# Optimization experiments

Measured on AMD Instinct MI355X. Metric: run time of the kernel, lower is better.

## Reference

```python
import jax, jax.numpy as jnp
import numpy as np

H_HEADS = 32
KV_HEADS = 8
HEAD_DIM = 64  # hidden // num_heads = 2048 // 32


def setup_inputs() -> dict:
    key = jax.random.key(0)
    ks = jax.random.split(key, 5)
    B, T, hidden = 2, 2048, 2048
    kv_dim = KV_HEADS * HEAD_DIM
    s = 0.02
    return {
        "x": jax.random.normal(ks[0], (B, T, hidden), dtype=jnp.float32),
        "Wq": jax.random.normal(ks[1], (hidden, hidden), dtype=jnp.float32) * s,
        "Wk": jax.random.normal(ks[2], (hidden, kv_dim), dtype=jnp.float32) * s,
        "Wv": jax.random.normal(ks[3], (hidden, kv_dim), dtype=jnp.float32) * s,
        "Wo": jax.random.normal(ks[4], (hidden, hidden), dtype=jnp.float32) * s,
    }


def reference(x, Wq, Wk, Wv, Wo):
    B, T, hidden = x.shape
    h, kv, d = H_HEADS, KV_HEADS, HEAD_DIM
    g = h // kv  # GQA group size
    scale = d ** (-0.5)

    # projections
    q = (x @ Wq).reshape(B, T, h, d).transpose(0, 2, 1, 3)        # [B,h,T,d]
    k = (x @ Wk).reshape(B, T, kv, d).transpose(0, 2, 1, 3)      # [B,kv,T,d]
    v = (x @ Wv).reshape(B, T, kv, d).transpose(0, 2, 1, 3)      # [B,kv,T,d]

    # native GQA broadcast: group q heads by their shared kv head
    # (equivalent math to torch repeat_interleave on k/v)
    qg = q.reshape(B, kv, g, T, d)                                # [B,kv,g,T,d]
    scores = jnp.einsum("bkgtd,bksd->bkgts", qg, k) * scale       # [B,kv,g,T,T]
    attn = jax.nn.softmax(scores, axis=-1)
    og = jnp.einsum("bkgts,bksd->bkgtd", attn, v)                 # [B,kv,g,T,d]
    out = og.reshape(B, h, T, d).transpose(0, 2, 1, 3).reshape(B, T, h * d)
    return out @ Wo
```

## Files before the change

kernel.cpp:

```cpp
#include <hip/hip_runtime.h>

#define AS1 __attribute__((address_space(1)))
#define AS3 __attribute__((address_space(3)))

typedef unsigned short u16;
typedef unsigned int u32;
typedef __attribute__((ext_vector_type(8))) _Float16 half8;
typedef __attribute__((ext_vector_type(2))) _Float16 half2v;
typedef __attribute__((ext_vector_type(4))) u16 u16x4;
typedef __attribute__((ext_vector_type(4))) u32 u32x4;
typedef __attribute__((ext_vector_type(4))) float f32x4;
typedef __attribute__((ext_vector_type(16))) float f32x16;

__device__ __forceinline__ u16 f2h(float f) {
    _Float16 h = (_Float16)f;
    return __builtin_bit_cast(u16, h);
}

__device__ __forceinline__ u32 pk2h(float a, float b) {
    return __builtin_bit_cast(u32, __builtin_amdgcn_cvt_pkrtz(a, b));
}

__device__ __forceinline__ float fexp2(float x) {
#if __has_builtin(__builtin_amdgcn_exp2f)
    return __builtin_amdgcn_exp2f(x);
#else
    return __expf(x * 0.69314718055994531f);
#endif
}

__device__ __forceinline__ float dot2acc(u32 w, float acc) {
#if __has_builtin(__builtin_amdgcn_fdot2)
    half2v ones = { (_Float16)1.f, (_Float16)1.f };
    return __builtin_amdgcn_fdot2(__builtin_bit_cast(half2v, w), ones, acc, false);
#else
    half2v p = __builtin_bit_cast(half2v, w);
    return acc + (float)p[0] + (float)p[1];
#endif
}

__device__ __forceinline__ void plswap(u32& a, u32& b) {
    asm("v_permlane32_swap_b32 %0, %1" : "+v"(a), "+v"(b));
}

__device__ __forceinline__ void async16(const void* g, void* l) {
    __builtin_amdgcn_global_load_lds((AS1 void*)g, (AS3 void*)l, 16, 0, 0);
}


__global__ void cast_f32_to_f16(const float* __restrict__ in, u16* __restrict__ out) {
    int i = (blockIdx.x * 256 + threadIdx.x) * 4;
    float4 v = *(const float4*)(in + i);
    u16x4 o = { f2h(v.x), f2h(v.y), f2h(v.z), f2h(v.w) };
    *(u16x4*)(out + i) = o;
}

__global__ void transpose_cast(const float* __restrict__ in, u16* __restrict__ out,
                               int K, int N, float scale) {
    __shared__ float tile[32][33];
    int nb = blockIdx.x * 32, kb = blockIdx.y * 32;
    int tx = threadIdx.x & 31, ty = threadIdx.x >> 5;
#pragma unroll
    for (int r = ty; r < 32; r += 8)
        tile[r][tx] = in[(size_t)(kb + r) * N + nb + tx];
    __syncthreads();
#pragma unroll
    for (int r = ty; r < 32; r += 8)
        out[(size_t)(nb + r) * K + kb + tx] = f2h(tile[tx][r] * scale);
}


template <int OUTMODE>
__global__ __launch_bounds__(256, OUTMODE == 3 ? 3 : 2) void gemm_bt(
        const u16* __restrict__ A, const u16* __restrict__ Bt,
        void* __restrict__ C, void* __restrict__ C2,
        int M, int N, int K, int ldc) {
    __shared__ __align__(16) u16 As[2][128 * 32];
    __shared__ __align__(16) u16 Bs[2][128 * 32];
    const int m0 = blockIdx.x * 128, n0 = blockIdx.y * 128;
    const int wave = threadIdx.x >> 6, lane = threadIdx.x & 63;
    const int quad = lane >> 4, mm = lane & 15;
    const int wm = (wave >> 1) * 64, wn = (wave & 1) * 64;

    const int srow = wave * 16 + (lane >> 2);
    const int scol = 8 * ((lane & 3) ^ ((lane >> 3) & 3));

    const u16* ag0 = A + (size_t)(m0 + srow) * K + scol;
    const u16* ag1 = A + (size_t)(m0 + 64 + srow) * K + scol;
    const u16* bg0 = Bt + (size_t)(n0 + srow) * K + scol;
    const u16* bg1 = Bt + (size_t)(n0 + 64 + srow) * K + scol;
    const int soff = wave * 512 + lane * 8;

    f32x4 acc[4][4] = {};
    const int swz = (mm >> 1) & 3;

#define GST(buf)                                                              \
    {                                                                         \
        u16* ad = &As[buf][soff];                                             \
        u16* bd = &Bs[buf][soff];                                             \
        async16(ag0, ad);                                                     \
        async16(ag1, ad + 2048);                                              \
        async16(bg0, bd);                                                     \
        async16(bg1, bd + 2048);                                              \
        ag0 += 32; ag1 += 32; bg0 += 32; bg1 += 32;                           \
    }

    GST(0);
    int cur = 0;

    for (int k0 = 0; k0 < K; k0 += 32) {
        __syncthreads();
        if (k0 + 32 < K) GST(cur ^ 1);
        const u16* Ac = &As[cur][0];
        const u16* Bc = &Bs[cur][0];
        half8 af[4], bf[4];
#pragma unroll
        for (int i = 0; i < 4; i++)
            af[i] = *(const half8*)(Ac + (wm + i * 16 + mm) * 32 + (quad ^ swz) * 8);
#pragma unroll
        for (int i = 0; i < 4; i++)
            bf[i] = *(const half8*)(Bc + (wn + i * 16 + mm) * 32 + (quad ^ swz) * 8);
#pragma unroll
        for (int mi = 0; mi < 4; mi++)
#pragma unroll
            for (int ni = 0; ni < 4; ni++)
                acc[mi][ni] = __builtin_amdgcn_mfma_f32_16x16x32_f16(
                    af[mi], bf[ni], acc[mi][ni], 0, 0, 0);
        cur ^= 1;
    }
#undef GST

    if (OUTMODE == 0) {
        float* Cp = (float*)C;
#pragma unroll
        for (int mi = 0; mi < 4; mi++)
#pragma unroll
            for (int r = 0; r < 4; r++) {
                float* rp = Cp + (size_t)(m0 + wm + mi * 16 + quad * 4 + r) * ldc + n0 + wn + mm;
#pragma unroll
                for (int ni = 0; ni < 4; ni++) rp[ni * 16] = acc[mi][ni][r];
            }
    } else if (OUTMODE == 1) {
        u16* Cp = (u16*)C;
#pragma unroll
        for (int mi = 0; mi < 4; mi++)
#pragma unroll
            for (int r = 0; r < 4; r++) {
                u16* rp = Cp + (size_t)(m0 + wm + mi * 16 + quad * 4 + r) * ldc + n0 + wn + mm;
#pragma unroll
                for (int ni = 0; ni < 4; ni++) rp[ni * 16] = f2h(acc[mi][ni][r]);
            }
    } else if (OUTMODE == 2) {
        u16* Cp = (u16*)C;
#pragma unroll
        for (int mi = 0; mi < 4; mi++)
#pragma unroll
            for (int r = 0; r < 4; r++) {
                int row = m0 + wm + mi * 16 + quad * 4 + r;
#pragma unroll
                for (int ni = 0; ni < 4; ni++)
                    Cp[(size_t)(n0 + wn + ni * 16 + mm) * ldc + row] = f2h(acc[mi][ni][r]);
            }
    } else {
        if (n0 < 2048) {
            u16* Qp = (u16*)C;
#pragma unroll
            for (int mi = 0; mi < 4; mi++)
#pragma unroll
                for (int r = 0; r < 4; r++) {
                    u16* rp = Qp + (size_t)(m0 + wm + mi * 16 + quad * 4 + r) * 2048 + n0 + wn + mm;
#pragma unroll
                    for (int ni = 0; ni < 4; ni++) rp[ni * 16] = f2h(acc[mi][ni][r]);
                }
        } else if (n0 < 2560) {
            u16* Kp = (u16*)C2;
#pragma unroll
            for (int mi = 0; mi < 4; mi++)
#pragma unroll
                for (int r = 0; r < 4; r++) {
                    u16* rp = Kp + (size_t)(m0 + wm + mi * 16 + quad * 4 + r) * 512 + (n0 - 2048) + wn + mm;
#pragma unroll
                    for (int ni = 0; ni < 4; ni++) rp[ni * 16] = f2h(acc[mi][ni][r]);
                }
        } else {
            u16* Vp = (u16*)C2 + (size_t)4096 * 512;
#pragma unroll
            for (int mi = 0; mi < 4; mi++)
#pragma unroll
                for (int r = 0; r < 4; r++) {
                    int row = m0 + wm + mi * 16 + quad * 4 + r;
#pragma unroll
                    for (int ni = 0; ni < 4; ni++)
                        Vp[(size_t)(n0 - 2560 + wn + ni * 16 + mm) * 4096 + row] = f2h(acc[mi][ni][r]);
                }
        }
    }
}


template <int SPLIT>
__global__ __launch_bounds__(256, 4) void attn_fwd(const u16* __restrict__ Qb,
                                                   const u16* __restrict__ Kb,
                                                   const u16* __restrict__ Vtb,
                                                   u16* __restrict__ Ob,
                                                   float* __restrict__ Of0,
                                                   float* __restrict__ Of1,
                                                   float* __restrict__ Lf) {
    __shared__ __align__(16) u16 Ks[2][64 * 64];
    __shared__ __align__(16) u16 Vs[2][64 * 64];

    const int qtb = blockIdx.x, head = blockIdx.y;
    const int b = blockIdx.z & 1, sp = blockIdx.z >> 1;
    const int kvh = head >> 2;
    const int wave = threadIdx.x >> 6, lane = threadIdx.x & 63;
    const int h = lane >> 5;
    const int q32 = lane & 31;
    const int t = threadIdx.x;

    const size_t qrow0 = (size_t)b * 2048 + qtb * 128 + wave * 32;
    const int s_beg = sp * (2048 / SPLIT), s_end = s_beg + 2048 / SPLIT;

    half8 qf[4];
#pragma unroll
    for (int s = 0; s < 4; s++)
        qf[s] = *(const half8*)(Qb + (qrow0 + q32) * 2048 + head * 64 + s * 16 + h * 8);

    f32x16 accO[2] = {};
    float lpq[4] = {0.f, 0.f, 0.f, 0.f};

    const int srow = t >> 3;
    const int lch = (t & 7) ^ (srow & 7);
    const u16* kg = Kb + ((size_t)b * 2048 + srow) * 512 + kvh * 64 + lch * 8;
    const u16* vg = Vtb + ((size_t)kvh * 64 + srow) * 4096 + b * 2048 + lch * 8;

#define STAGE(buf, s0)                                                        \
    {                                                                         \
        u16* kd = &Ks[buf][t * 8];                                            \
        u16* vd = &Vs[buf][t * 8];                                            \
        async16(kg + (size_t)(s0) * 512, kd);                                 \
        async16(kg + (size_t)((s0) + 32) * 512, kd + 2048);                   \
        async16(vg + (s0), vd);                                               \
        async16(vg + (size_t)32 * 4096 + (s0), vd + 2048);                    \
    }

    int cur = 0;
    STAGE(0, s_beg);

    const int r0 = q32, r1 = 32 + q32;
    const int sw0 = (r0 & 7), sw1 = (r1 & 7);

    for (int s0 = s_beg; s0 < s_end; s0 += 64) {
        __syncthreads();
        int sn = s0 + 64;
        if (sn < s_end) STAGE(cur ^ 1, sn);

        const u16* Kc = &Ks[cur][0];
        const u16* Vc = &Vs[cur][0];
        const u16* Kr0 = Kc + r0 * 64;
        const u16* Kr1 = Kc + r1 * 64;

        f32x16 a0, a1;
#pragma unroll
        for (int i = 0; i < 16; i++) { a0[i] = -10.f; a1[i] = -10.f; }

#pragma unroll
        for (int s = 0; s < 4; s++) {
            half8 k0 = *(const half8*)(Kr0 + (((2 * s + h) ^ sw0) << 3));
            a0 = __builtin_amdgcn_mfma_f32_32x32x16_f16(k0, qf[s], a0, 0, 0, 0);
            half8 k1 = *(const half8*)(Kr1 + (((2 * s + h) ^ sw1) << 3));
            a1 = __builtin_amdgcn_mfma_f32_32x32x16_f16(k1, qf[s], a1, 0, 0, 0);
        }

        u32 w0[8];
#pragma unroll
        for (int m = 0; m < 8; m++) {
            w0[m] = pk2h(fexp2(a0[2 * m]), fexp2(a0[2 * m + 1]));
            lpq[m & 3] = dot2acc(w0[m], lpq[m & 3]);
        }

#pragma unroll
        for (int k1 = 0; k1 < 2; k1++) {
            const int ks = k1;
            u32 d0 = w0[4 * k1 + 0], d2 = w0[4 * k1 + 2];
            u32 d1 = w0[4 * k1 + 1], d3 = w0[4 * k1 + 3];
            plswap(d0, d2);
            plswap(d1, d3);
            u32x4 pd = { d0, d1, d2, d3 };
            half8 pf = __builtin_bit_cast(half8, pd);
#pragma unroll
            for (int dt = 0; dt < 2; dt++) {
                const int rv = dt * 32 + q32;
                half8 vf = *(const half8*)(&Vc[rv * 64 + (((2 * ks + h) ^ (rv & 7)) << 3)]);
                accO[dt] = __builtin_amdgcn_mfma_f32_32x32x16_f16(vf, pf, accO[dt], 0, 0, 0);
            }
        }

        u32 w1[8];
#pragma unroll
        for (int m = 0; m < 8; m++) {
            w1[m] = pk2h(fexp2(a1[2 * m]), fexp2(a1[2 * m + 1]));
            lpq[m & 3] = dot2acc(w1[m], lpq[m & 3]);
        }

#pragma unroll
        for (int k1 = 0; k1 < 2; k1++) {
            const int ks = 2 + k1;
            u32 d0 = w1[4 * k1 + 0], d2 = w1[4 * k1 + 2];
            u32 d1 = w1[4 * k1 + 1], d3 = w1[4 * k1 + 3];
            plswap(d0, d2);
            plswap(d1, d3);
            u32x4 pd = { d0, d1, d2, d3 };
            half8 pf = __builtin_bit_cast(half8, pd);
#pragma unroll
            for (int dt = 0; dt < 2; dt++) {
                const int rv = dt * 32 + q32;
                half8 vf = *(const half8*)(&Vc[rv * 64 + (((2 * ks + h) ^ (rv & 7)) << 3)]);
                accO[dt] = __builtin_amdgcn_mfma_f32_32x32x16_f16(vf, pf, accO[dt], 0, 0, 0);
            }
        }

        cur ^= 1;
    }
#undef STAGE

    float l = (lpq[0] + lpq[1]) + (lpq[2] + lpq[3]);
    l += __shfl_xor(l, 32);

    const size_t token = qrow0 + q32;
    if (SPLIT == 1) {
        float inv = 1.f / l;
#pragma unroll
        for (int dt = 0; dt < 2; dt++)
#pragma unroll
            for (int rq = 0; rq < 4; rq++) {
                u16x4 o = { f2h(accO[dt][4 * rq + 0] * inv), f2h(accO[dt][4 * rq + 1] * inv),
                            f2h(accO[dt][4 * rq + 2] * inv), f2h(accO[dt][4 * rq + 3] * inv) };
                *(u16x4*)(Ob + token * 2048 + head * 64 + dt * 32 + rq * 8 + h * 4) = o;
            }
    } else {
        float* Op = sp ? Of1 : Of0;
#pragma unroll
        for (int dt = 0; dt < 2; dt++)
#pragma unroll
            for (int rq = 0; rq < 4; rq++) {
                f32x4 o = { accO[dt][4 * rq + 0], accO[dt][4 * rq + 1],
                            accO[dt][4 * rq + 2], accO[dt][4 * rq + 3] };
                *(f32x4*)(Op + token * 2048 + head * 64 + dt * 32 + rq * 8 + h * 4) = o;
            }
        if (!h) Lf[((size_t)sp * 4096 + token) * 32 + head] = l;
    }
}


extern "C" void kernel_launch(void* const* d_in, const int* in_sizes, int n_in,
                              void* d_out, int out_size, void* d_ws, size_t ws_size,
                              hipStream_t stream) {
    (void)in_sizes; (void)n_in; (void)out_size; (void)ws_size;
    const float* x  = (const float*)d_in[0];
    const float* Wq = (const float*)d_in[1];
    const float* Wk = (const float*)d_in[2];
    const float* Wv = (const float*)d_in[3];
    const float* Wo = (const float*)d_in[4];
    float* out = (float*)d_out;

    u16* ws = (u16*)d_ws;
    u16* xb   = ws;
    u16* Wqt  = xb   + (size_t)4096 * 2048;
    u16* Wkvt = Wqt  + (size_t)2048 * 2048;
    u16* Wot  = Wkvt + (size_t)1024 * 2048;
    u16* Qb   = Wot  + (size_t)2048 * 2048;
    u16* Kb   = Qb   + (size_t)4096 * 2048;
    u16* Vtb  = Kb   + (size_t)4096 * 512;
    u16* Ob   = Vtb  + (size_t)512 * 4096;

    const float qscale = 0.125f * 1.4426950408889634f;

    cast_f32_to_f16<<<8192, 256, 0, stream>>>(x, xb);
    transpose_cast<<<dim3(64, 64), 256, 0, stream>>>(Wq, Wqt, 2048, 2048, qscale);
    transpose_cast<<<dim3(16, 64), 256, 0, stream>>>(Wk, Wkvt, 2048, 512, 1.f);
    transpose_cast<<<dim3(16, 64), 256, 0, stream>>>(Wv, Wkvt + (size_t)512 * 2048, 2048, 512, 1.f);
    transpose_cast<<<dim3(64, 64), 256, 0, stream>>>(Wo, Wot, 2048, 2048, 1.f);

    gemm_bt<3><<<dim3(32, 24), 256, 0, stream>>>(xb, Wqt, Qb, Kb, 4096, 3072, 2048, 2048);

    attn_fwd<1><<<dim3(16, 32, 2), 256, 0, stream>>>(Qb, Kb, Vtb, Ob,
                                                     nullptr, nullptr, nullptr);

    gemm_bt<0><<<dim3(32, 16), 256, 0, stream>>>(Ob, Wot, out, nullptr, 4096, 2048, 2048, 2048);
}
```

Baseline: 312.1 us.

## Split attention over keys with combine pass, merge weight transposes, add MFMA priority

Attention now runs as a two-way split over the key range, which doubles the grid to improve occupancy. Partial fp32 outputs and row sums go to the output buffer and extra workspace, and a new combine kernel merges them into fp16. The four weight transpose launches become one launch indexed by grid z. The attention kernel also raises its launch-bound occupancy hint, seeds the first score MFMA directly from a constant, and wraps the MFMA blocks in s_setprio. The split path needs enough workspace, falls back to the old path otherwise, and adds extra fp32 traffic plus a combine launch.

```diff
diff --git a/kernel.cpp b/kernel.cpp
--- a/kernel.cpp
+++ b/kernel.cpp
@@ -55,10 +55,23 @@
     *(u16x4*)(out + i) = o;
 }
 
-__global__ void transpose_cast(const float* __restrict__ in, u16* __restrict__ out,
-                               int K, int N, float scale) {
+__global__ void transpose_cast4(const float* __restrict__ Wq, const float* __restrict__ Wk,
+                                const float* __restrict__ Wv, const float* __restrict__ Wo,
+                                u16* __restrict__ Wqt, u16* __restrict__ Wkvt,
+                                u16* __restrict__ Wot, float qscale) {
     __shared__ float tile[32][33];
+    const int z = blockIdx.z;
+    const float* in;
+    u16* out;
+    int N;
+    float scale = 1.f;
+    if (z == 0)      { in = Wq; out = Wqt; N = 2048; scale = qscale; }
+    else if (z == 1) { in = Wo; out = Wot; N = 2048; }
+    else if (z == 2) { in = Wk; out = Wkvt; N = 512; }
+    else             { in = Wv; out = Wkvt + (size_t)512 * 2048; N = 512; }
+    const int K = 2048;
     int nb = blockIdx.x * 32, kb = blockIdx.y * 32;
+    if (nb >= N) return;
     int tx = threadIdx.x & 31, ty = threadIdx.x >> 5;
 #pragma unroll
     for (int r = ty; r < 32; r += 8)
@@ -199,7 +212,7 @@
 
 
 template <int SPLIT>
-__global__ __launch_bounds__(256, 4) void attn_fwd(const u16* __restrict__ Qb,
+__global__ __launch_bounds__(256, 5) void attn_fwd(const u16* __restrict__ Qb,
                                                    const u16* __restrict__ Kb,
                                                    const u16* __restrict__ Vtb,
                                                    u16* __restrict__ Ob,
@@ -228,6 +241,10 @@
     f32x16 accO[2] = {};
     float lpq[4] = {0.f, 0.f, 0.f, 0.f};
 
+    f32x16 NEG10;
+#pragma unroll
+    for (int i = 0; i < 16; i++) NEG10[i] = -10.f;
+
     const int srow = t >> 3;
     const int lch = (t & 7) ^ (srow & 7);
     const u16* kg = Kb + ((size_t)b * 2048 + srow) * 512 + kvh * 64 + lch * 8;
@@ -260,16 +277,21 @@
         const u16* Kr1 = Kc + r1 * 64;
 
         f32x16 a0, a1;
-#pragma unroll
-        for (int i = 0; i < 16; i++) { a0[i] = -10.f; a1[i] = -10.f; }
-
-#pragma unroll
-        for (int s = 0; s < 4; s++) {
+        __builtin_amdgcn_s_setprio(1);
+        {
+            half8 k0 = *(const half8*)(Kr0 + ((h ^ sw0) << 3));
+            a0 = __builtin_amdgcn_mfma_f32_32x32x16_f16(k0, qf[0], NEG10, 0, 0, 0);
+            half8 k1 = *(const half8*)(Kr1 + ((h ^ sw1) << 3));
+            a1 = __builtin_amdgcn_mfma_f32_32x32x16_f16(k1, qf[0], NEG10, 0, 0, 0);
+        }
+#pragma unroll
+        for (int s = 1; s < 4; s++) {
             half8 k0 = *(const half8*)(Kr0 + (((2 * s + h) ^ sw0) << 3));
             a0 = __builtin_amdgcn_mfma_f32_32x32x16_f16(k0, qf[s], a0, 0, 0, 0);
             half8 k1 = *(const half8*)(Kr1 + (((2 * s + h) ^ sw1) << 3));
             a1 = __builtin_amdgcn_mfma_f32_32x32x16_f16(k1, qf[s], a1, 0, 0, 0);
         }
+        __builtin_amdgcn_s_setprio(0);
 
         u32 w0[8];
 #pragma unroll
@@ -278,6 +300,7 @@
             lpq[m & 3] = dot2acc(w0[m], lpq[m & 3]);
         }
 
+        __builtin_amdgcn_s_setprio(1);
 #pragma unroll
         for (int k1 = 0; k1 < 2; k1++) {
             const int ks = k1;
@@ -294,6 +317,7 @@
                 accO[dt] = __builtin_amdgcn_mfma_f32_32x32x16_f16(vf, pf, accO[dt], 0, 0, 0);
             }
         }
+        __builtin_amdgcn_s_setprio(0);
 
         u32 w1[8];
 #pragma unroll
@@ -302,6 +326,7 @@
             lpq[m & 3] = dot2acc(w1[m], lpq[m & 3]);
         }
 
+        __builtin_amdgcn_s_setprio(1);
 #pragma unroll
         for (int k1 = 0; k1 < 2; k1++) {
             const int ks = 2 + k1;
@@ -318,6 +343,7 @@
                 accO[dt] = __builtin_amdgcn_mfma_f32_32x32x16_f16(vf, pf, accO[dt], 0, 0, 0);
             }
         }
+        __builtin_amdgcn_s_setprio(0);
 
         cur ^= 1;
     }
@@ -351,11 +377,25 @@
     }
 }
 
+__global__ void attn_combine(const float* __restrict__ Of0, const float* __restrict__ Of1,
+                             const float* __restrict__ Lf, u16* __restrict__ Ob) {
+    size_t idx = (size_t)blockIdx.x * 256 + threadIdx.x;
+    size_t token = idx >> 9;
+    int dq = (int)(idx & 511) * 4;
+    int head = dq >> 6;
+    float inv = 1.f / (Lf[token * 32 + head] + Lf[(4096 + token) * 32 + head]);
+    float4 a = *(const float4*)(Of0 + token * 2048 + dq);
+    float4 c = *(const float4*)(Of1 + token * 2048 + dq);
+    u16x4 o = { f2h((a.x + c.x) * inv), f2h((a.y + c.y) * inv),
+                f2h((a.z + c.z) * inv), f2h((a.w + c.w) * inv) };
+    *(u16x4*)(Ob + token * 2048 + dq) = o;
+}
+
 
 extern "C" void kernel_launch(void* const* d_in, const int* in_sizes, int n_in,
                               void* d_out, int out_size, void* d_ws, size_t ws_size,
                               hipStream_t stream) {
-    (void)in_sizes; (void)n_in; (void)out_size; (void)ws_size;
+    (void)in_sizes; (void)n_in; (void)out_size;
     const float* x  = (const float*)d_in[0];
     const float* Wq = (const float*)d_in[1];
     const float* Wk = (const float*)d_in[2];
@@ -372,19 +412,27 @@
     u16* Kb   = Qb   + (size_t)4096 * 2048;
     u16* Vtb  = Kb   + (size_t)4096 * 512;
     u16* Ob   = Vtb  + (size_t)512 * 4096;
+    u16* wend = Ob   + (size_t)4096 * 2048;
+    float* Of1 = (float*)wend;
+    float* Lf  = (float*)((char*)Of1 + (size_t)4096 * 2048 * 4);
+    size_t need = (size_t)((char*)Lf - (char*)d_ws) + (size_t)2 * 4096 * 32 * 4;
+    const bool split = ws_size >= need;
 
     const float qscale = 0.125f * 1.4426950408889634f;
 
     cast_f32_to_f16<<<8192, 256, 0, stream>>>(x, xb);
-    transpose_cast<<<dim3(64, 64), 256, 0, stream>>>(Wq, Wqt, 2048, 2048, qscale);
-    transpose_cast<<<dim3(16, 64), 256, 0, stream>>>(Wk, Wkvt, 2048, 512, 1.f);
-    transpose_cast<<<dim3(16, 64), 256, 0, stream>>>(Wv, Wkvt + (size_t)512 * 2048, 2048, 512, 1.f);
-    transpose_cast<<<dim3(64, 64), 256, 0, stream>>>(Wo, Wot, 2048, 2048, 1.f);
+    transpose_cast4<<<dim3(64, 64, 4), 256, 0, stream>>>(Wq, Wk, Wv, Wo,
+                                                         Wqt, Wkvt, Wot, qscale);
 
     gemm_bt<3><<<dim3(32, 24), 256, 0, stream>>>(xb, Wqt, Qb, Kb, 4096, 3072, 2048, 2048);
 
-    attn_fwd<1><<<dim3(16, 32, 2), 256, 0, stream>>>(Qb, Kb, Vtb, Ob,
-                                                     nullptr, nullptr, nullptr);
+    if (split) {
+        attn_fwd<2><<<dim3(16, 32, 4), 256, 0, stream>>>(Qb, Kb, Vtb, Ob, out, Of1, Lf);
+        attn_combine<<<8192, 256, 0, stream>>>(out, Of1, Lf, Ob);
+    } else {
+        attn_fwd<1><<<dim3(16, 32, 2), 256, 0, stream>>>(Qb, Kb, Vtb, Ob,
+                                                         nullptr, nullptr, nullptr);
+    }
 
     gemm_bt<0><<<dim3(32, 16), 256, 0, stream>>>(Ob, Wot, out, nullptr, 4096, 2048, 2048, 2048);
 }
```

New measurement: 401.7 us. 1.29x slower.
